# Optimization experiments

Measured on AMD Instinct MI355X. Metric: run time of the kernel, lower is better.

The kernel has to match this reference:

```python
import jax, jax.numpy as jnp
import numpy as np

EPS = 1e-12  # matches torch F.normalize eps clamp


def _l2norm(v, axis):
    n = jnp.sqrt(jnp.sum(v * v, axis=axis, keepdims=True))
    return v / jnp.maximum(n, EPS)


def setup_inputs() -> dict:
    key = jax.random.key(0)
    k1, k2, k3, k4 = jax.random.split(key, 4)
    N, C, H, W, K = 64, 128, 64, 64, 64
    x = jax.random.normal(k1, (N, C, H, W), dtype=jnp.float32)
    conv_w = jax.random.normal(k2, (K, C), dtype=jnp.float32) * 0.1  # 1x1 conv weight squeezed
    conv_b = jax.random.normal(k3, (K,), dtype=jnp.float32) * 0.1
    centroids = jax.random.uniform(k4, (K, C), dtype=jnp.float32)
    return {"x": x, "conv_w": conv_w, "conv_b": conv_b, "centroids": centroids}


def reference(x, conv_w, conv_b, centroids):
    N, C = x.shape[:2]
    K = centroids.shape[0]
    xf = x.reshape(N, C, -1)                                   # (N, C, P) with P = H*W
    # 1x1 conv == per-pixel linear map over channels
    logits = jnp.einsum('ncp,kc->nkp', xf, conv_w) + conv_b[None, :, None]
    a = jax.nn.softmax(logits, axis=1)                         # soft assignment over clusters
    # vlad[n,k,c] = sum_p a[n,k,p] * (x[n,c,p] - centroids[k,c])
    vlad = jnp.einsum('nkp,ncp->nkc', a, xf) \
        - jnp.sum(a, axis=-1)[:, :, None] * centroids[None]    # (N, K, C)
    vlad = _l2norm(vlad, axis=2)                               # intra-cluster normalization
    vlad = vlad.reshape(N, K * C)
    return _l2norm(vlad, axis=1)
```

## Files before the change

kernel.cpp:

```cpp
#include <hip/hip_runtime.h>
#include <math.h>

#define NNIMG 64
#define CCH 128
#define KK 64
#define PP 4096
#define BSPLIT 16
#define PB 256
#define PC 32
#define NCHUNK (PB / PC)

typedef __attribute__((ext_vector_type(8))) short short8;
typedef __attribute__((ext_vector_type(4))) float f32x4;

__device__ __forceinline__ unsigned short bf16_rtne(float f) {
  unsigned u = __float_as_uint(f);
  unsigned r = u + 0x7FFFu + ((u >> 16) & 1u);
  return (unsigned short)(r >> 16);
}
__device__ __forceinline__ float bf16_tof(unsigned short h) {
  return __uint_as_float(((unsigned)h) << 16);
}
__device__ __forceinline__ void lgkm_barrier() {
  __asm__ volatile("s_waitcnt lgkmcnt(0)\n\ts_barrier" ::: "memory");
}

template <bool USE_WS>
__global__ __launch_bounds__(128, 2) void netvlad_main(
    const float* __restrict__ x, const float* __restrict__ conv_w,
    const float* __restrict__ conv_b, float* __restrict__ vout,
    float* __restrict__ aout) {
  __shared__ __align__(16) unsigned int pc[2][PC * 66];
  __shared__ __align__(16) unsigned short a_lds[KK * 40];
  __shared__ float asum_buf[2 * KK];

  const int t = threadIdx.x;
  const int lane = t & 63;
  const int wv = t >> 6;
  const int m = lane & 15;
  const int q = lane >> 4;

  const int n = blockIdx.x >> 4;
  const int blk = blockIdx.x & 15;
  const float* xbase = x + (size_t)n * CCH * PP + blk * PB;

  const int lrow = lane >> 3;
  const int lpx = (lane & 7) * 4;
  f32x4 sreg[8];
  auto issue_loads = [&](int ch) {
#pragma unroll
    for (int j = 0; j < 8; ++j) {
      const int row = wv * 64 + (j >> 1) * 16 + lrow * 2 + (j & 1);
      sreg[j] = *(const f32x4*)(xbase + (size_t)row * PP + ch * PC + lpx);
    }
  };

  issue_loads(0);

  short8 Whi[4][4];
#pragma unroll
  for (int kt = 0; kt < 4; ++kt)
#pragma unroll
    for (int cs = 0; cs < 4; ++cs) {
      const float* wp = conv_w + (kt * 16 + m) * CCH + cs * 32 + q * 8;
      float4 wa = *(const float4*)wp;
      float4 wb = *(const float4*)(wp + 4);
      float fv[8] = {wa.x, wa.y, wa.z, wa.w, wb.x, wb.y, wb.z, wb.w};
      short8 h;
#pragma unroll
      for (int j = 0; j < 8; ++j) h[j] = (short)bf16_rtne(fv[j]);
      Whi[kt][cs] = h;
    }
  float b_regs[4][4];
#pragma unroll
  for (int kt = 0; kt < 4; ++kt)
#pragma unroll
    for (int r = 0; r < 4; ++r) b_regs[kt][r] = conv_b[kt * 16 + q * 4 + r];

  f32x4 vacc[4][4];
#pragma unroll
  for (int kt = 0; kt < 4; ++kt)
#pragma unroll
    for (int ct = 0; ct < 4; ++ct) vacc[kt][ct] = (f32x4){0.f, 0.f, 0.f, 0.f};
  float asum_acc[16];
#pragma unroll
  for (int i = 0; i < 16; ++i) asum_acc[i] = 0.f;

  const int prow = wv * 16 + m;
  const unsigned sel_hi = 0x07060302u;
  const unsigned sel_g2 = (m & 1) ? 0x07060302u : 0x05040100u;

#pragma unroll 1
  for (int ch = 0; ch < NCHUNK; ++ch) {
    unsigned int* pcb = pc[ch & 1];

#pragma unroll
    for (int u = 0; u < 4; ++u) {
      const int e = wv * 32 + u * 8 + lrow;
      f32x4 ev = sreg[2 * u];
      f32x4 od = sreg[2 * u + 1];
#pragma unroll
      for (int pi = 0; pi < 4; ++pi)
        pcb[(lpx + pi) * 66 + e] =
            __builtin_amdgcn_perm(__float_as_uint(od[pi]), __float_as_uint(ev[pi]), sel_hi);
    }
    if (ch + 1 < NCHUNK) issue_loads(ch + 1);
    lgkm_barrier();

    f32x4 acc1[4];
#pragma unroll
    for (int kt = 0; kt < 4; ++kt)
      acc1[kt] = (f32x4){b_regs[kt][0], b_regs[kt][1], b_regs[kt][2], b_regs[kt][3]};
    const unsigned int* pcrow = pcb + prow * 66;
#pragma unroll
    for (int cs = 0; cs < 4; ++cs) {
      uint2 u01 = *(const uint2*)&pcrow[16 * cs + 4 * q];
      uint2 u23 = *(const uint2*)&pcrow[16 * cs + 4 * q + 2];
      unsigned hs[4] = {u01.x, u01.y, u23.x, u23.y};
      short8 Bf;
      __builtin_memcpy(&Bf, hs, 16);
#pragma unroll
      for (int kt = 0; kt < 4; ++kt)
        acc1[kt] = __builtin_amdgcn_mfma_f32_16x16x32_bf16(Whi[kt][cs], Bf, acc1[kt], 0, 0, 0);
    }

    float ssum = 0.f;
#pragma unroll
    for (int kt = 0; kt < 4; ++kt)
#pragma unroll
      for (int r = 0; r < 4; ++r) {
        float e = __expf(acc1[kt][r]);
        acc1[kt][r] = e;
        ssum += e;
      }
    ssum += __shfl_xor(ssum, 16, 64);
    ssum += __shfl_xor(ssum, 32, 64);
    float inv = 1.0f / ssum;
#pragma unroll
    for (int kt = 0; kt < 4; ++kt)
#pragma unroll
      for (int r = 0; r < 4; ++r) {
        float a = acc1[kt][r] * inv;
        unsigned short h = bf16_rtne(a);
        asum_acc[kt * 4 + r] += bf16_tof(h);
        a_lds[(kt * 16 + q * 4 + r) * 40 + prow] = h;
      }
    lgkm_barrier();

    short8 Af[4];
#pragma unroll
    for (int kt = 0; kt < 4; ++kt)
      Af[kt] = *(const short8*)&a_lds[(kt * 16 + m) * 40 + q * 8];
#pragma unroll
    for (int ct = 0; ct < 4; ++ct) {
      const int ebase = wv * 32 + ct * 8 + (m >> 1);
      unsigned g[8];
#pragma unroll
      for (int j = 0; j < 8; ++j) g[j] = pcb[(q * 8 + j) * 66 + ebase];
      unsigned hs2[4];
#pragma unroll
      for (int i = 0; i < 4; ++i)
        hs2[i] = __builtin_amdgcn_perm(g[2 * i + 1], g[2 * i], sel_g2);
      short8 Bf;
      __builtin_memcpy(&Bf, hs2, 16);
#pragma unroll
      for (int kt = 0; kt < 4; ++kt)
        vacc[kt][ct] = __builtin_amdgcn_mfma_f32_16x16x32_bf16(Af[kt], Bf, vacc[kt][ct], 0, 0, 0);
    }
  }

  float* vrow = USE_WS ? (vout + (size_t)blockIdx.x * (KK * CCH))
                       : (vout + (size_t)n * (KK * CCH));
#pragma unroll
  for (int kt = 0; kt < 4; ++kt)
#pragma unroll
    for (int ct = 0; ct < 4; ++ct)
#pragma unroll
      for (int r = 0; r < 4; ++r) {
        const int idx = (kt * 16 + q * 4 + r) * CCH + wv * 64 + ct * 16 + m;
        if (USE_WS) vrow[idx] = vacc[kt][ct][r];
        else atomicAdd(&vrow[idx], vacc[kt][ct][r]);
      }
#pragma unroll
  for (int i = 0; i < 16; ++i) {
    float v = asum_acc[i];
    v += __shfl_xor(v, 1, 64);
    v += __shfl_xor(v, 2, 64);
    v += __shfl_xor(v, 4, 64);
    v += __shfl_xor(v, 8, 64);
    if (m == 0) asum_buf[wv * 64 + (i >> 2) * 16 + q * 4 + (i & 3)] = v;
  }
  lgkm_barrier();
  if (t < KK) {
    float s = asum_buf[t] + asum_buf[KK + t];
    if (USE_WS) aout[blockIdx.x * KK + t] = s;
    else atomicAdd(&aout[n * KK + t], s);
  }
}

__global__ __launch_bounds__(256) void netvlad_finish(
    const float* __restrict__ vg, const float* __restrict__ ag,
    const float* __restrict__ centroids, float* __restrict__ out) {
  const int t = threadIdx.x;
  const int w = t >> 6, ln = t & 63;
  const int idx = blockIdx.x * 4 + w;
  const int n = idx >> 6, k = idx & 63;
  const int c = ln * 2;
  float2 v = *(const float2*)&vg[(size_t)(n * KK + k) * CCH + c];
  float s = ag[n * KK + k];
  float2 ce = *(const float2*)&centroids[k * CCH + c];
  float v0 = v.x - s * ce.x;
  float v1 = v.y - s * ce.y;
  float ssq = v0 * v0 + v1 * v1;
#pragma unroll
  for (int off = 32; off > 0; off >>= 1) ssq += __shfl_xor(ssq, off, 64);
  float inv = 0.125f / fmaxf(sqrtf(ssq), 1e-12f);
  float2 o;
  o.x = v0 * inv;
  o.y = v1 * inv;
  *(float2*)&out[(size_t)n * (KK * CCH) + k * CCH + c] = o;
}

__global__ __launch_bounds__(256) void netvlad_finish_ws(
    const float* __restrict__ vp, const float* __restrict__ agp,
    const float* __restrict__ centroids, float* __restrict__ out) {
  const int t = threadIdx.x;
  const int w = t >> 6, ln = t & 63;
  const int idx = blockIdx.x * 4 + w;
  const int n = idx >> 6, k = idx & 63;
  const int c = ln * 2;
  float a0 = 0.f, a1 = 0.f, s = 0.f;
#pragma unroll
  for (int b = 0; b < BSPLIT; ++b) {
    const float* vr = vp + (size_t)(n * BSPLIT + b) * (KK * CCH) + k * CCH + c;
    float2 v = *(const float2*)vr;
    a0 += v.x;
    a1 += v.y;
    s += agp[(n * BSPLIT + b) * KK + k];
  }
  float2 ce = *(const float2*)&centroids[k * CCH + c];
  float v0 = a0 - s * ce.x;
  float v1 = a1 - s * ce.y;
  float ssq = v0 * v0 + v1 * v1;
#pragma unroll
  for (int off = 32; off > 0; off >>= 1) ssq += __shfl_xor(ssq, off, 64);
  float inv = 0.125f / fmaxf(sqrtf(ssq), 1e-12f);
  float2 o;
  o.x = v0 * inv;
  o.y = v1 * inv;
  *(float2*)&out[(size_t)n * (KK * CCH) + k * CCH + c] = o;
}

extern "C" void kernel_launch(void* const* d_in, const int* in_sizes, int n_in,
                              void* d_out, int out_size, void* d_ws, size_t ws_size,
                              hipStream_t stream) {
  const float* x = (const float*)d_in[0];
  const float* conv_w = (const float*)d_in[1];
  const float* conv_b = (const float*)d_in[2];
  const float* centroids = (const float*)d_in[3];
  float* out = (float*)d_out;

  const size_t WS_NEEDED =
      ((size_t)NNIMG * BSPLIT * KK * CCH + (size_t)NNIMG * BSPLIT * KK) * sizeof(float);

  if (ws_size >= WS_NEEDED) {
    float* vp = (float*)d_ws;
    float* agp = vp + (size_t)NNIMG * BSPLIT * KK * CCH;
    netvlad_main<true><<<NNIMG * BSPLIT, 128, 0, stream>>>(x, conv_w, conv_b, vp, agp);
    netvlad_finish_ws<<<NNIMG * KK / 4, 256, 0, stream>>>(vp, agp, centroids, out);
  } else {
    float* vg = (float*)d_ws;
    float* ag = vg + (size_t)NNIMG * KK * CCH;
    const size_t zbytes = ((size_t)NNIMG * KK * CCH + NNIMG * KK) * sizeof(float);
    hipMemsetAsync(d_ws, 0, zbytes, stream);
    netvlad_main<false><<<NNIMG * BSPLIT, 128, 0, stream>>>(x, conv_w, conv_b, vg, ag);
    netvlad_finish<<<NNIMG * KK / 4, 256, 0, stream>>>(vg, ag, centroids, out);
  }
}
```

Measured before the change: 217.2 us.

## Fold centroid subtraction into main kernel and atomically accumulate into output

The main kernel now subtracts the per-block assignment sum times the centroids itself, and atomically adds its partial VLAD tile straight into the zeroed output buffer. A small in-place kernel then applies the intra-cluster and global normalization. This removes the 16-way partial workspace write and read-back and the separate reduction pass. In exchange it adds a memset and float atomic contention (16 blocks per image hitting the same addresses), and the summation order becomes nondeterministic.

```diff
diff --git a/kernel.cpp b/kernel.cpp
--- a/kernel.cpp
+++ b/kernel.cpp
@@ -25,11 +25,10 @@
   __asm__ volatile("s_waitcnt lgkmcnt(0)\n\ts_barrier" ::: "memory");
 }
 
-template <bool USE_WS>
 __global__ __launch_bounds__(128, 2) void netvlad_main(
     const float* __restrict__ x, const float* __restrict__ conv_w,
-    const float* __restrict__ conv_b, float* __restrict__ vout,
-    float* __restrict__ aout) {
+    const float* __restrict__ conv_b, const float* __restrict__ centroids,
+    float* __restrict__ out) {
   __shared__ __align__(16) unsigned int pc[2][PC * 66];
   __shared__ __align__(16) unsigned short a_lds[KK * 40];
   __shared__ float asum_buf[2 * KK];
@@ -169,18 +168,6 @@
     }
   }
 
-  float* vrow = USE_WS ? (vout + (size_t)blockIdx.x * (KK * CCH))
-                       : (vout + (size_t)n * (KK * CCH));
-#pragma unroll
-  for (int kt = 0; kt < 4; ++kt)
-#pragma unroll
-    for (int ct = 0; ct < 4; ++ct)
-#pragma unroll
-      for (int r = 0; r < 4; ++r) {
-        const int idx = (kt * 16 + q * 4 + r) * CCH + wv * 64 + ct * 16 + m;
-        if (USE_WS) vrow[idx] = vacc[kt][ct][r];
-        else atomicAdd(&vrow[idx], vacc[kt][ct][r]);
-      }
 #pragma unroll
   for (int i = 0; i < 16; ++i) {
     float v = asum_acc[i];
@@ -191,64 +178,41 @@
     if (m == 0) asum_buf[wv * 64 + (i >> 2) * 16 + q * 4 + (i & 3)] = v;
   }
   lgkm_barrier();
-  if (t < KK) {
-    float s = asum_buf[t] + asum_buf[KK + t];
-    if (USE_WS) aout[blockIdx.x * KK + t] = s;
-    else atomicAdd(&aout[n * KK + t], s);
+  float s_k[16];
+#pragma unroll
+  for (int i = 0; i < 16; ++i) {
+    const int k = (i >> 2) * 16 + q * 4 + (i & 3);
+    s_k[i] = asum_buf[k] + asum_buf[KK + k];
   }
-}
-
-__global__ __launch_bounds__(256) void netvlad_finish(
-    const float* __restrict__ vg, const float* __restrict__ ag,
-    const float* __restrict__ centroids, float* __restrict__ out) {
+  float* orow = out + (size_t)n * (KK * CCH);
+#pragma unroll
+  for (int kt = 0; kt < 4; ++kt)
+#pragma unroll
+    for (int ct = 0; ct < 4; ++ct)
+#pragma unroll
+      for (int r = 0; r < 4; ++r) {
+        const int k = kt * 16 + q * 4 + r;
+        const int c = wv * 64 + ct * 16 + m;
+        const float v = vacc[kt][ct][r] - s_k[kt * 4 + r] * centroids[k * CCH + c];
+        atomicAdd(&orow[k * CCH + c], v);
+      }
+}
+
+__global__ __launch_bounds__(256) void netvlad_norm(float* __restrict__ out) {
   const int t = threadIdx.x;
   const int w = t >> 6, ln = t & 63;
   const int idx = blockIdx.x * 4 + w;
-  const int n = idx >> 6, k = idx & 63;
+  float* vr = out + (size_t)idx * CCH;
   const int c = ln * 2;
-  float2 v = *(const float2*)&vg[(size_t)(n * KK + k) * CCH + c];
-  float s = ag[n * KK + k];
-  float2 ce = *(const float2*)&centroids[k * CCH + c];
-  float v0 = v.x - s * ce.x;
-  float v1 = v.y - s * ce.y;
-  float ssq = v0 * v0 + v1 * v1;
+  float2 v = *(const float2*)&vr[c];
+  float ssq = v.x * v.x + v.y * v.y;
 #pragma unroll
   for (int off = 32; off > 0; off >>= 1) ssq += __shfl_xor(ssq, off, 64);
   float inv = 0.125f / fmaxf(sqrtf(ssq), 1e-12f);
   float2 o;
-  o.x = v0 * inv;
-  o.y = v1 * inv;
-  *(float2*)&out[(size_t)n * (KK * CCH) + k * CCH + c] = o;
-}
-
-__global__ __launch_bounds__(256) void netvlad_finish_ws(
-    const float* __restrict__ vp, const float* __restrict__ agp,
-    const float* __restrict__ centroids, float* __restrict__ out) {
-  const int t = threadIdx.x;
-  const int w = t >> 6, ln = t & 63;
-  const int idx = blockIdx.x * 4 + w;
-  const int n = idx >> 6, k = idx & 63;
-  const int c = ln * 2;
-  float a0 = 0.f, a1 = 0.f, s = 0.f;
-#pragma unroll
-  for (int b = 0; b < BSPLIT; ++b) {
-    const float* vr = vp + (size_t)(n * BSPLIT + b) * (KK * CCH) + k * CCH + c;
-    float2 v = *(const float2*)vr;
-    a0 += v.x;
-    a1 += v.y;
-    s += agp[(n * BSPLIT + b) * KK + k];
-  }
-  float2 ce = *(const float2*)&centroids[k * CCH + c];
-  float v0 = a0 - s * ce.x;
-  float v1 = a1 - s * ce.y;
-  float ssq = v0 * v0 + v1 * v1;
-#pragma unroll
-  for (int off = 32; off > 0; off >>= 1) ssq += __shfl_xor(ssq, off, 64);
-  float inv = 0.125f / fmaxf(sqrtf(ssq), 1e-12f);
-  float2 o;
-  o.x = v0 * inv;
-  o.y = v1 * inv;
-  *(float2*)&out[(size_t)n * (KK * CCH) + k * CCH + c] = o;
+  o.x = v.x * inv;
+  o.y = v.y * inv;
+  *(float2*)&vr[c] = o;
 }
 
 extern "C" void kernel_launch(void* const* d_in, const int* in_sizes, int n_in,
@@ -260,20 +224,10 @@
   const float* centroids = (const float*)d_in[3];
   float* out = (float*)d_out;
 
-  const size_t WS_NEEDED =
-      ((size_t)NNIMG * BSPLIT * KK * CCH + (size_t)NNIMG * BSPLIT * KK) * sizeof(float);
-
-  if (ws_size >= WS_NEEDED) {
-    float* vp = (float*)d_ws;
-    float* agp = vp + (size_t)NNIMG * BSPLIT * KK * CCH;
-    netvlad_main<true><<<NNIMG * BSPLIT, 128, 0, stream>>>(x, conv_w, conv_b, vp, agp);
-    netvlad_finish_ws<<<NNIMG * KK / 4, 256, 0, stream>>>(vp, agp, centroids, out);
-  } else {
-    float* vg = (float*)d_ws;
-    float* ag = vg + (size_t)NNIMG * KK * CCH;
-    const size_t zbytes = ((size_t)NNIMG * KK * CCH + NNIMG * KK) * sizeof(float);
-    hipMemsetAsync(d_ws, 0, zbytes, stream);
-    netvlad_main<false><<<NNIMG * BSPLIT, 128, 0, stream>>>(x, conv_w, conv_b, vg, ag);
-    netvlad_finish<<<NNIMG * KK / 4, 256, 0, stream>>>(vg, ag, centroids, out);
-  }
-}
+  (void)d_ws;
+  (void)ws_size;
+
+  hipMemsetAsync(d_out, 0, (size_t)NNIMG * KK * CCH * sizeof(float), stream);
+  netvlad_main<<<NNIMG * BSPLIT, 128, 0, stream>>>(x, conv_w, conv_b, centroids, out);
+  netvlad_norm<<<NNIMG * KK / 4, 256, 0, stream>>>(out);
+}
```

New measurement: 242.4 us. +11.6%, slower.
